# Performance work log

Measured on AMD Instinct MI355X. Metric: run time of the kernel, lower is better.

The kernel has to match this reference:

```python
import jax, jax.numpy as jnp
import numpy as np

N_NODES = 100000
N_EDGES = 3200000
IN_F = 256
OUT_F = 256


def setup_inputs() -> dict:
    key = jax.random.key(0)
    k1, k2, k3, k4, k5, k6 = jax.random.split(key, 6)
    x = jax.random.normal(k1, (N_NODES, IN_F), dtype=jnp.float32)
    edge_row = jnp.sort(jax.random.randint(k2, (N_EDGES,), 0, N_NODES, dtype=jnp.int64))
    edge_col = jax.random.randint(k3, (N_EDGES,), 0, N_NODES, dtype=jnp.int64)
    edge_val = jax.random.uniform(k4, (N_EDGES,), dtype=jnp.float32)
    stdv = 1.0 / np.sqrt(OUT_F)
    weight = jax.random.uniform(k5, (IN_F, OUT_F), dtype=jnp.float32, minval=-stdv, maxval=stdv)
    bias = jax.random.uniform(k6, (OUT_F,), dtype=jnp.float32, minval=-stdv, maxval=stdv)
    return {"x": x, "edge_row": edge_row, "edge_col": edge_col,
            "edge_val": edge_val, "weight": weight, "bias": bias}


def reference(x, edge_row, edge_col, edge_val, weight, bias):
    # support = x @ W  -> [N, out]
    support = jnp.matmul(x, weight)
    # spmm(adj, support): out[r] = sum_e val[e] * support[col[e]] for edges with row[e]==r
    gathered = support[edge_col] * edge_val[:, None]  # [E, out]
    output = jax.ops.segment_sum(gathered, edge_row, num_segments=N_NODES)
    return output + bias
```

## Files before the change

kernel.cpp:

```cpp
#include <hip/hip_runtime.h>
#include <hip/hip_bf16.h>

#define NN 100000
#define NE 3200000
#define NF 256
#define CHUNK 512
#define GEMM_BLOCKS 1250
#define RP_BLOCKS   1563

typedef __attribute__((ext_vector_type(8))) __bf16 bf16x8;
typedef __attribute__((ext_vector_type(4))) float  f32x4;
typedef __attribute__((ext_vector_type(4))) int    i32x4;


__global__ __launch_bounds__(256) void prep_w(const float* __restrict__ w,
                                              __bf16* __restrict__ wfrag,
                                              const float* __restrict__ bias,
                                              float* __restrict__ bias_p) {
    if (blockIdx.x == 32) {
        const int t = threadIdx.x;
        const int l = t >> 2, b = t & 3;
        bias_p[t] = bias[(l & 3) * 64 + 16 * b + (l >> 2)];
        return;
    }
    const int t = blockIdx.x * 256 + threadIdx.x;
    const int lane = t & 63;
    const int nf   = (t >> 6) & 15;
    const int ks   = t >> 10;
    const int col  = nf * 16 + (lane & 15);
    const int k0   = ks * 32 + (lane >> 4) * 8;
    bf16x8 v;
#pragma unroll
    for (int j = 0; j < 8; ++j) v[j] = (__bf16)w[(k0 + j) * NF + col];
    reinterpret_cast<bf16x8*>(wfrag)[t] = v;
}

__global__ __launch_bounds__(320) void gemm_q(const float* __restrict__ x,
                                              const __bf16* __restrict__ wfrag,
                                              unsigned char* __restrict__ tab,
                                              float* __restrict__ scales,
                                              const int* __restrict__ erow,
                                              int* __restrict__ rowptr) {
    if (blockIdx.x >= GEMM_BLOCKS) {
        const int t8 = (blockIdx.x - GEMM_BLOCKS) * 320 + threadIdx.x;
        if (t8 >= NE / 8) return;
        const int base = t8 * 8;
        const i32x4 c0 = *reinterpret_cast<const i32x4*>(erow + base);
        const i32x4 c1 = *reinterpret_cast<const i32x4*>(erow + base + 4);
        const int E[8] = {c0.x, c0.y, c0.z, c0.w, c1.x, c1.y, c1.z, c1.w};
        int prev = (base == 0) ? -1 : erow[base - 1];
#pragma unroll
        for (int j = 0; j < 8; ++j) {
            const int r = E[j];
            for (int q = prev + 1; q <= r; ++q) rowptr[q] = base + j;
            prev = r;
        }
        if (base + 8 == NE) {
            for (int q = prev + 1; q <= NN; ++q) rowptr[q] = NE;
        }
        return;
    }

    __shared__ __align__(16) __bf16 As[80 * 72];
    __shared__ __align__(16) bf16x8 Bs[2048];

    const int t    = threadIdx.x;
    const int wv   = t >> 6;
    const int lane = t & 63;
    const int row0 = blockIdx.x * 80;

    f32x4 acc[16];
#pragma unroll
    for (int nf = 0; nf < 16; ++nf) acc[nf] = (f32x4){0.f, 0.f, 0.f, 0.f};

    const int    srow = t >> 2;
    const int    sc   = (t & 3) * 16;
    const float* xp   = x + (size_t)(row0 + srow) * NF + sc;
    char* const  wr   = reinterpret_cast<char*>(As) + srow * 144 + sc * 2;

    const char* const rd =
        reinterpret_cast<const char*>(As) + (wv * 16 + (lane & 15)) * 144 + ((lane >> 4) << 4);

    const bf16x8* wf = reinterpret_cast<const bf16x8*>(wfrag);

    f32x4 s0 = __builtin_nontemporal_load(reinterpret_cast<const f32x4*>(xp));
    f32x4 s1 = __builtin_nontemporal_load(reinterpret_cast<const f32x4*>(xp + 4));
    f32x4 s2 = __builtin_nontemporal_load(reinterpret_cast<const f32x4*>(xp + 8));
    f32x4 s3 = __builtin_nontemporal_load(reinterpret_cast<const f32x4*>(xp + 12));

    for (int p = 0; p < 4; ++p) {
        for (int i = t; i < 2048; i += 320) Bs[i] = wf[p * 2048 + i];

        bf16x8 b0, b1;
        b0[0] = (__bf16)s0.x; b0[1] = (__bf16)s0.y; b0[2] = (__bf16)s0.z; b0[3] = (__bf16)s0.w;
        b0[4] = (__bf16)s1.x; b0[5] = (__bf16)s1.y; b0[6] = (__bf16)s1.z; b0[7] = (__bf16)s1.w;
        b1[0] = (__bf16)s2.x; b1[1] = (__bf16)s2.y; b1[2] = (__bf16)s2.z; b1[3] = (__bf16)s2.w;
        b1[4] = (__bf16)s3.x; b1[5] = (__bf16)s3.y; b1[6] = (__bf16)s3.z; b1[7] = (__bf16)s3.w;
        *reinterpret_cast<bf16x8*>(wr)      = b0;
        *reinterpret_cast<bf16x8*>(wr + 16) = b1;
        __syncthreads();

        if (p < 3) {
            const float* nx = xp + (p + 1) * 64;
            s0 = __builtin_nontemporal_load(reinterpret_cast<const f32x4*>(nx));
            s1 = __builtin_nontemporal_load(reinterpret_cast<const f32x4*>(nx + 4));
            s2 = __builtin_nontemporal_load(reinterpret_cast<const f32x4*>(nx + 8));
            s3 = __builtin_nontemporal_load(reinterpret_cast<const f32x4*>(nx + 12));
        }

        const bf16x8 af0 = *reinterpret_cast<const bf16x8*>(rd);
        const bf16x8 af1 = *reinterpret_cast<const bf16x8*>(rd + 64);
#pragma unroll
        for (int nf = 0; nf < 16; ++nf) {
            const bf16x8 w0 = Bs[(0 * 16 + nf) * 64 + lane];
            acc[nf] = __builtin_amdgcn_mfma_f32_16x16x32_bf16(af0, w0, acc[nf], 0, 0, 0);
        }
#pragma unroll
        for (int nf = 0; nf < 16; ++nf) {
            const bf16x8 w1 = Bs[(1 * 16 + nf) * 64 + lane];
            acc[nf] = __builtin_amdgcn_mfma_f32_16x16x32_bf16(af1, w1, acc[nf], 0, 0, 0);
        }
        __syncthreads();
    }

    const int hi   = lane >> 4;
    const int ccol = lane & 15;

    float m[4];
#pragma unroll
    for (int r = 0; r < 4; ++r) {
        float mm = 0.f;
#pragma unroll
        for (int nf = 0; nf < 16; ++nf) mm = fmaxf(mm, fabsf(acc[nf][r]));
        m[r] = mm;
    }
#pragma unroll
    for (int w = 1; w < 16; w <<= 1) {
#pragma unroll
        for (int r = 0; r < 4; ++r) m[r] = fmaxf(m[r], __shfl_xor(m[r], w, 64));
    }

#pragma unroll
    for (int r = 0; r < 4; ++r) {
        const int   node = row0 + wv * 16 + hi * 4 + r;
        const float isc  = 127.0f / fmaxf(m[r], 1e-30f);
        uint4 pk = {0u, 0u, 0u, 0u};
        unsigned int* pw = reinterpret_cast<unsigned int*>(&pk);
#pragma unroll
        for (int nf = 0; nf < 16; ++nf) {
            const int q = (int)rintf(acc[nf][r] * isc) + 128;
            pw[nf >> 2] |= ((unsigned int)(q & 0xff)) << ((nf & 3) * 8);
        }
        *reinterpret_cast<uint4*>(tab + (size_t)node * 256 + ccol * 16) = pk;
        if (ccol == 0) scales[node] = m[r] * (1.0f / 127.0f);
    }
}

__global__ __launch_bounds__(256) void spmm_f(const unsigned int* __restrict__ tab32,
                                              const int* __restrict__ rowptr,
                                              const int* __restrict__ ecol,
                                              const float* __restrict__ eval,
                                              const float* __restrict__ scales,
                                              const float* __restrict__ bias_p,
                                              float* __restrict__ out) {
    __shared__ int2 buf[CHUNK];

    const int wave = threadIdx.x >> 6;
    const int lane = threadIdx.x & 63;
    const int row  = blockIdx.x * 4 + wave;

    const int bs   = rowptr[blockIdx.x * 4];
    const int bend = rowptr[blockIdx.x * 4 + 4];
    const int rs   = rowptr[row];
    const int re   = rowptr[row + 1];

    float a0 = 0.f, a1 = 0.f, a2 = 0.f, a3 = 0.f, S = 0.f;

    for (int cs = bs; cs < bend; cs += CHUNK) {
        const int cnt = min(CHUNK, bend - cs);
        if (cs != bs) __syncthreads();
        for (int j = threadIdx.x; j < cnt; j += 256) {
            const int   c = ecol[cs + j];
            const float v = eval[cs + j];
            buf[j] = make_int2(c, __float_as_int(v * scales[c]));
        }
        __syncthreads();

        const int lo = max(rs, cs);
        const int hi = min(re, cs + cnt);
#pragma unroll 4
        for (int i = lo; i < hi; ++i) {
            const int2  p = buf[i - cs];
            const float v = __int_as_float(p.y);
            const unsigned int g = tab32[((unsigned)p.x << 6) + lane];
            a0 = fmaf(v, (float)(g & 0xffu), a0);
            a1 = fmaf(v, (float)((g >> 8) & 0xffu), a1);
            a2 = fmaf(v, (float)((g >> 16) & 0xffu), a2);
            a3 = fmaf(v, (float)(g >> 24), a3);
            S += v;
        }
    }

    const f32x4 bp = *reinterpret_cast<const f32x4*>(bias_p + lane * 4);
    const float c128 = 128.0f * S;
    float* op = out + (size_t)row * NF + (lane & 3) * 64 + (lane >> 2);
    __builtin_nontemporal_store(a0 - c128 + bp.x, op);
    __builtin_nontemporal_store(a1 - c128 + bp.y, op + 16);
    __builtin_nontemporal_store(a2 - c128 + bp.z, op + 32);
    __builtin_nontemporal_store(a3 - c128 + bp.w, op + 48);
}

extern "C" void kernel_launch(void* const* d_in, const int* in_sizes, int n_in,
                              void* d_out, int out_size, void* d_ws, size_t ws_size,
                              hipStream_t stream) {
    const float* x    = (const float*)d_in[0];
    const int*   erow = (const int*)d_in[1];
    const int*   ecol = (const int*)d_in[2];
    const float* eval = (const float*)d_in[3];
    const float* w    = (const float*)d_in[4];
    const float* bias = (const float*)d_in[5];
    float*       out  = (float*)d_out;

    unsigned char* tab    = (unsigned char*)d_ws;
    int*           rowptr = (int*)((char*)d_ws + 25600000);
    __bf16*        wfrag  = (__bf16*)((char*)d_ws + 26000016);
    float*         scales = (float*)((char*)d_ws + 26131088);
    float*         bias_p = (float*)((char*)d_ws + 26531088);

    prep_w<<<33, 256, 0, stream>>>(w, wfrag, bias, bias_p);
    gemm_q<<<GEMM_BLOCKS + RP_BLOCKS, 320, 0, stream>>>(x, wfrag, tab, scales,
                                                        erow, rowptr);
    spmm_f<<<NN / 4, 256, 0, stream>>>(
        reinterpret_cast<const unsigned int*>(tab), rowptr, ecol, eval, scales,
        bias_p, out);
}
```

Baseline: 180.7 us.

## Shard quantized feature table into column slices so SpMM gathers fit in cache

The int8 support table is rewritten as 8 column shards of 32 bytes per node. The SpMM grid grows 8x so each block handles one shard for 4 rows, and each wave processes 8 edges at once with 8 lanes each, followed by a shuffle reduction. Each shard is about 3.2MB, so the intent is for the random gathers of a shard to stay resident in cache rather than hitting HBM. The cost is that edge indices and values, plus the scales lookup, are re-read 8 times, and the grid has many more blocks. Bias permutation is dropped and bias is read directly.

```diff
diff --git a/kernel.cpp b/kernel.cpp
--- a/kernel.cpp
+++ b/kernel.cpp
@@ -10,19 +10,12 @@
 
 typedef __attribute__((ext_vector_type(8))) __bf16 bf16x8;
 typedef __attribute__((ext_vector_type(4))) float  f32x4;
+typedef __attribute__((ext_vector_type(2))) float  f32x2;
 typedef __attribute__((ext_vector_type(4))) int    i32x4;
 
 
 __global__ __launch_bounds__(256) void prep_w(const float* __restrict__ w,
-                                              __bf16* __restrict__ wfrag,
-                                              const float* __restrict__ bias,
-                                              float* __restrict__ bias_p) {
-    if (blockIdx.x == 32) {
-        const int t = threadIdx.x;
-        const int l = t >> 2, b = t & 3;
-        bias_p[t] = bias[(l & 3) * 64 + 16 * b + (l >> 2)];
-        return;
-    }
+                                              __bf16* __restrict__ wfrag) {
     const int t = blockIdx.x * 256 + threadIdx.x;
     const int lane = t & 63;
     const int nf   = (t >> 6) & 15;
@@ -37,7 +30,7 @@
 
 __global__ __launch_bounds__(320) void gemm_q(const float* __restrict__ x,
                                               const __bf16* __restrict__ wfrag,
-                                              unsigned char* __restrict__ tab,
+                                              unsigned char* __restrict__ tabS,
                                               float* __restrict__ scales,
                                               const int* __restrict__ erow,
                                               int* __restrict__ rowptr) {
@@ -144,35 +137,43 @@
     for (int r = 0; r < 4; ++r) {
         const int   node = row0 + wv * 16 + hi * 4 + r;
         const float isc  = 127.0f / fmaxf(m[r], 1e-30f);
-        uint4 pk = {0u, 0u, 0u, 0u};
-        unsigned int* pw = reinterpret_cast<unsigned int*>(&pk);
-#pragma unroll
-        for (int nf = 0; nf < 16; ++nf) {
-            const int q = (int)rintf(acc[nf][r] * isc) + 128;
-            pw[nf >> 2] |= ((unsigned int)(q & 0xff)) << ((nf & 3) * 8);
-        }
-        *reinterpret_cast<uint4*>(tab + (size_t)node * 256 + ccol * 16) = pk;
+        unsigned int qb[16];
+#pragma unroll
+        for (int nf = 0; nf < 16; ++nf)
+            qb[nf] = (unsigned int)(((int)rintf(acc[nf][r] * isc) + 128) & 0xff);
+#pragma unroll
+        for (int sh = 0; sh < 8; ++sh) {
+            const unsigned short u16v = (unsigned short)(qb[sh] | (qb[sh + 8] << 8));
+            *reinterpret_cast<unsigned short*>(
+                tabS + ((size_t)sh * NN + node) * 32 + ccol * 2) = u16v;
+        }
         if (ccol == 0) scales[node] = m[r] * (1.0f / 127.0f);
     }
 }
 
-__global__ __launch_bounds__(256) void spmm_f(const unsigned int* __restrict__ tab32,
+__global__ __launch_bounds__(256) void spmm_s(const unsigned char* __restrict__ tabS,
                                               const int* __restrict__ rowptr,
                                               const int* __restrict__ ecol,
                                               const float* __restrict__ eval,
                                               const float* __restrict__ scales,
-                                              const float* __restrict__ bias_p,
+                                              const float* __restrict__ bias,
                                               float* __restrict__ out) {
     __shared__ int2 buf[CHUNK];
 
+    const int sh   = blockIdx.x & 7;
+    const int rg   = blockIdx.x >> 3;
     const int wave = threadIdx.x >> 6;
     const int lane = threadIdx.x & 63;
-    const int row  = blockIdx.x * 4 + wave;
-
-    const int bs   = rowptr[blockIdx.x * 4];
-    const int bend = rowptr[blockIdx.x * 4 + 4];
+    const int g    = lane >> 3;
+    const int u    = lane & 7;
+    const int row  = rg * 4 + wave;
+
+    const int bs   = rowptr[rg * 4];
+    const int bend = rowptr[rg * 4 + 4];
     const int rs   = rowptr[row];
     const int re   = rowptr[row + 1];
+
+    const unsigned char* ts = tabS + (size_t)sh * NN * 32;
 
     float a0 = 0.f, a1 = 0.f, a2 = 0.f, a3 = 0.f, S = 0.f;
 
@@ -180,34 +181,49 @@
         const int cnt = min(CHUNK, bend - cs);
         if (cs != bs) __syncthreads();
         for (int j = threadIdx.x; j < cnt; j += 256) {
-            const int   c = ecol[cs + j];
-            const float v = eval[cs + j];
+            const int   c = __builtin_nontemporal_load(ecol + cs + j);
+            const float v = __builtin_nontemporal_load(eval + cs + j);
             buf[j] = make_int2(c, __float_as_int(v * scales[c]));
         }
         __syncthreads();
 
         const int lo = max(rs, cs);
         const int hi = min(re, cs + cnt);
-#pragma unroll 4
-        for (int i = lo; i < hi; ++i) {
-            const int2  p = buf[i - cs];
-            const float v = __int_as_float(p.y);
-            const unsigned int g = tab32[((unsigned)p.x << 6) + lane];
-            a0 = fmaf(v, (float)(g & 0xffu), a0);
-            a1 = fmaf(v, (float)((g >> 8) & 0xffu), a1);
-            a2 = fmaf(v, (float)((g >> 16) & 0xffu), a2);
-            a3 = fmaf(v, (float)(g >> 24), a3);
+#pragma unroll 2
+        for (int i = lo; i < hi; i += 8) {
+            const int  idx = i + g;
+            const bool act = idx < hi;
+            const int2 p = buf[(act ? idx : lo) - cs];
+            const float v = act ? __int_as_float(p.y) : 0.f;
+            const unsigned int gg = *reinterpret_cast<const unsigned int*>(
+                ts + (size_t)(unsigned)p.x * 32 + u * 4);
+            a0 = fmaf(v, (float)(gg & 0xffu), a0);
+            a1 = fmaf(v, (float)((gg >> 8) & 0xffu), a1);
+            a2 = fmaf(v, (float)((gg >> 16) & 0xffu), a2);
+            a3 = fmaf(v, (float)(gg >> 24), a3);
             S += v;
         }
     }
 
-    const f32x4 bp = *reinterpret_cast<const f32x4*>(bias_p + lane * 4);
-    const float c128 = 128.0f * S;
-    float* op = out + (size_t)row * NF + (lane & 3) * 64 + (lane >> 2);
-    __builtin_nontemporal_store(a0 - c128 + bp.x, op);
-    __builtin_nontemporal_store(a1 - c128 + bp.y, op + 16);
-    __builtin_nontemporal_store(a2 - c128 + bp.z, op + 32);
-    __builtin_nontemporal_store(a3 - c128 + bp.w, op + 48);
+#pragma unroll
+    for (int d = 8; d < 64; d <<= 1) {
+        a0 += __shfl_xor(a0, d, 64);
+        a1 += __shfl_xor(a1, d, 64);
+        a2 += __shfl_xor(a2, d, 64);
+        a3 += __shfl_xor(a3, d, 64);
+        S  += __shfl_xor(S,  d, 64);
+    }
+
+    if (lane < 8) {
+        const float c128 = 128.0f * S;
+        const int f0 = sh * 16 + 2 * u;
+        const int f1 = (sh + 8) * 16 + 2 * u;
+        f32x2 o0, o1;
+        o0.x = a0 - c128 + bias[f0];  o0.y = a2 - c128 + bias[f0 + 1];
+        o1.x = a1 - c128 + bias[f1];  o1.y = a3 - c128 + bias[f1 + 1];
+        __builtin_nontemporal_store(o0, reinterpret_cast<f32x2*>(out + (size_t)row * NF + f0));
+        __builtin_nontemporal_store(o1, reinterpret_cast<f32x2*>(out + (size_t)row * NF + f1));
+    }
 }
 
 extern "C" void kernel_launch(void* const* d_in, const int* in_sizes, int n_in,
@@ -221,16 +237,14 @@
     const float* bias = (const float*)d_in[5];
     float*       out  = (float*)d_out;
 
-    unsigned char* tab    = (unsigned char*)d_ws;
+    unsigned char* tabS   = (unsigned char*)d_ws;
     int*           rowptr = (int*)((char*)d_ws + 25600000);
     __bf16*        wfrag  = (__bf16*)((char*)d_ws + 26000016);
     float*         scales = (float*)((char*)d_ws + 26131088);
-    float*         bias_p = (float*)((char*)d_ws + 26531088);
-
-    prep_w<<<33, 256, 0, stream>>>(w, wfrag, bias, bias_p);
-    gemm_q<<<GEMM_BLOCKS + RP_BLOCKS, 320, 0, stream>>>(x, wfrag, tab, scales,
+
+    prep_w<<<32, 256, 0, stream>>>(w, wfrag);
+    gemm_q<<<GEMM_BLOCKS + RP_BLOCKS, 320, 0, stream>>>(x, wfrag, tabS, scales,
                                                         erow, rowptr);
-    spmm_f<<<NN / 4, 256, 0, stream>>>(
-        reinterpret_cast<const unsigned int*>(tab), rowptr, ecol, eval, scales,
-        bias_p, out);
-}
+    spmm_s<<<8 * (NN / 4), 256, 0, stream>>>(tabS, rowptr, ecol, eval, scales,
+                                             bias, out);
+}
```

New measurement: 421.9 us. 133% more time.
